# Kernel optimization log

Hardware: AMD Instinct MI355X
Metric: run time of the kernel (lower is better)

The kernel has to match this reference:

```python
import jax, jax.numpy as jnp
import numpy as np

NUM_EMBEDDINGS = 1024
EMBEDDING_DIM = 128
COMMITMENT_COEF = 0.25
DECAY = 0.99
EPS = 1e-5


def setup_inputs() -> dict:
    key = jax.random.key(0)
    k1, k2 = jax.random.split(key)
    z_e = jax.random.normal(k1, (64, EMBEDDING_DIM, 32, 32), dtype=jnp.float32)
    lim = 1.0 / NUM_EMBEDDINGS
    embed = jax.random.uniform(k2, (NUM_EMBEDDINGS, EMBEDDING_DIM), dtype=jnp.float32,
                               minval=-lim, maxval=lim)
    ema_cluster_size = jnp.zeros((NUM_EMBEDDINGS,), dtype=jnp.float32)
    ema_w = embed.copy()  # buffer initialized as clone of embed weights
    return {"z_e": z_e, "embed": embed,
            "ema_cluster_size": ema_cluster_size, "ema_w": ema_w}


def reference(z_e, embed, ema_cluster_size, ema_w):
    B, D, H, W = z_e.shape
    K = embed.shape[0]
    # [B,D,H,W] -> [N,D]
    flat = jnp.transpose(z_e, (0, 2, 3, 1)).reshape(-1, D)
    distances = (jnp.sum(flat ** 2, axis=1, keepdims=True)
                 + jnp.sum(embed ** 2, axis=1)
                 - 2.0 * jnp.matmul(flat, embed.T))
    encoding_indices = jnp.argmin(distances, axis=1)  # [N]

    quantized = embed[encoding_indices].reshape(B, H, W, D)
    quantized = jnp.transpose(quantized, (0, 3, 1, 2))  # [B,D,H,W]

    # ---- EMA codebook update (training path) ----
    N = flat.shape[0]
    cluster_size = jax.ops.segment_sum(jnp.ones((N,), flat.dtype),
                                       encoding_indices, num_segments=K)
    new_ema_cluster_size = DECAY * ema_cluster_size + (1.0 - DECAY) * cluster_size
    dw = jax.ops.segment_sum(flat, encoding_indices, num_segments=K)  # encodings^T @ flat
    new_ema_w = DECAY * ema_w + (1.0 - DECAY) * dw
    n = jnp.sum(new_ema_cluster_size)
    cs = (new_ema_cluster_size + EPS) / (n + K * EPS) * n
    new_embed = new_ema_w / cs[:, None]

    commitment_loss = jnp.mean((jax.lax.stop_gradient(quantized) - z_e) ** 2)
    loss = commitment_loss * COMMITMENT_COEF
    # straight-through estimator
    quantized_st = z_e + jax.lax.stop_gradient(quantized - z_e)
    indices = encoding_indices.reshape(B, H * W)
    return (quantized_st, indices, loss, new_embed, new_ema_cluster_size, new_ema_w)
```

## Files before the change

### kernel.cpp

```cpp
#include <hip/hip_runtime.h>

#define K_CODES 1024
#define DIM 128
#define HW 1024
#define NTOT 65536
#define DECAY 0.99f
#define OMD 0.01f
#define EPS 1e-5f
#define CCOEF 0.25f
#define MARGIN 1e-4f
#define FLCAP 24576

#define OFF_Q    0
#define OFF_IDX  8388608
#define OFF_LOSS (8388608 + 65536)
#define OFF_EMB  (OFF_LOSS + 1)
#define OFF_ECS  (OFF_EMB + 131072)
#define OFF_EMAW (OFF_ECS + 1024)

#define W_NORM2 0
#define W_RCP   1024
#define W_HIST  2048
#define W_LOSS  3072
#define W_FLCNT 3073
#define W_CNT2  3076
#define W_FL    (3076 + 24576)
#define W_M1F   (27652 + 24576)
#define W_CAND  (52228 + 24576)
#define W_EH    (76804 + 196608)
#define W_EL    (273412 + 65536)
#define W_NXIDX (338948 + 65536)
#define W_FLAT  (404484 + 65536)
#define W_NEED  (470020 + 8388608)

typedef __attribute__((ext_vector_type(8))) short short8v;
typedef __attribute__((ext_vector_type(4))) float f32x4;

__device__ __forceinline__ unsigned short f2bf(float f) {
    unsigned u = __float_as_uint(f);
    u += 0x7fffu + ((u >> 16) & 1u);
    return (unsigned short)(u >> 16);
}
__device__ __forceinline__ float bf2f(unsigned short h) {
    return __uint_as_float(((unsigned)h) << 16);
}

__global__ __launch_bounds__(256) void kzero(float* __restrict__ p, int n) {
    int i = blockIdx.x * 256 + threadIdx.x;
    if (i < n) p[i] = 0.f;
}

__device__ __forceinline__ float np_pairwise_sumsq_128(const float* p, size_t stride) {
    float r[8][4];
    #pragma unroll
    for (int j = 0; j < 8; ++j)
        #pragma unroll
        for (int L = 0; L < 4; ++L) {
            float x = p[(size_t)(j * 4 + L) * stride];
            r[j][L] = __fmul_rn(x, x);
        }
    #pragma unroll
    for (int c = 1; c < 4; ++c)
        #pragma unroll
        for (int j = 0; j < 8; ++j)
            #pragma unroll
            for (int L = 0; L < 4; ++L) {
                float x = p[(size_t)(c * 32 + j * 4 + L) * stride];
                r[j][L] = __fadd_rn(r[j][L], __fmul_rn(x, x));
            }
    float V[4];
    #pragma unroll
    for (int L = 0; L < 4; ++L) {
        float a = __fadd_rn(r[0][L], r[1][L]);
        float b = __fadd_rn(r[2][L], r[3][L]);
        float c2 = __fadd_rn(r[4][L], r[5][L]);
        float d2 = __fadd_rn(r[6][L], r[7][L]);
        V[L] = __fadd_rn(__fadd_rn(a, b), __fadd_rn(c2, d2));
    }
    return __fadd_rn(__fadd_rn(V[0], V[1]), __fadd_rn(V[2], V[3]));
}

__global__ __launch_bounds__(256) void knx(const float* __restrict__ ze,
                                           float* __restrict__ nx,
                                           float* __restrict__ flat_c) {
    __shared__ float t[128][133];
    const int tid = threadIdx.x;
    const int n0 = blockIdx.x * 128;
    const int b = n0 >> 10, hw0 = n0 & (HW - 1);
    const float* zb = ze + (size_t)b * (DIM * HW) + hw0;
    #pragma unroll
    for (int i = 0; i < 64; ++i) {
        int d = i * 2 + (tid >> 7);
        int hw = tid & 127;
        t[hw][d] = zb[(size_t)d * HW + hw];
    }
    __syncthreads();
    if (tid < 128) nx[n0 + tid] = np_pairwise_sumsq_128(&t[tid][0], 1);
    if (flat_c) {
        #pragma unroll
        for (int i = 0; i < 16; ++i) {
            int lin = i * 256 + tid;
            int r  = lin >> 5;
            int c4 = lin & 31;
            float4 v = *(const float4*)&t[r][c4 * 4];
            *(float4*)&flat_c[(size_t)(n0 + r) * DIM + c4 * 4] = v;
        }
    }
}

__global__ __launch_bounds__(256) void knorm(const float* __restrict__ embed,
                                             float* __restrict__ norm2,
                                             unsigned short* __restrict__ eh_g,
                                             unsigned short* __restrict__ el_g) {
    int k = blockIdx.x * 256 + threadIdx.x;
    const float* row = embed + (size_t)k * DIM;
    norm2[k] = np_pairwise_sumsq_128(row, 1);
    if (eh_g) {
        #pragma unroll 8
        for (int d = 0; d < DIM; ++d) {
            float f = row[d];
            unsigned short h = f2bf(f);
            eh_g[(size_t)k * DIM + d] = h;
            el_g[(size_t)k * DIM + d] = f2bf(f - bf2f(h));
        }
    }
}

__global__ __launch_bounds__(256, 4) void kapprox(
    const float* __restrict__ flat_c, const unsigned short* __restrict__ eh_g,
    const unsigned short* __restrict__ el_g, const float* __restrict__ norm2,
    int* __restrict__ idx_ws, float* __restrict__ idx_out,
    unsigned* __restrict__ hist, unsigned* __restrict__ flcnt,
    unsigned* __restrict__ fl_list, float* __restrict__ m1f)
{
    __shared__ __align__(16) unsigned short ehs[2][32 * 128];
    __shared__ __align__(16) unsigned short els[2][32 * 128];
    __shared__ float nes[1024];

    const int tid = threadIdx.x;
    const int l = tid & 63;
    const int w = tid >> 6;
    const int lg = l >> 4;
    const int lm = l & 15;
    const int n0 = blockIdx.x * 64;

    for (int i = tid; i < 1024; i += 256) nes[i] = norm2[i];

    short8v xh[4], xl[4];
    {
        const float* xr = flat_c + (size_t)(n0 + w * 16 + lm) * DIM;
        #pragma unroll
        for (int ks = 0; ks < 4; ++ks) {
            int kb = ks * 32 + lg * 8;
            float f0[8];
            *(float4*)&f0[0] = *(const float4*)(xr + kb);
            *(float4*)&f0[4] = *(const float4*)(xr + kb + 4);
            #pragma unroll
            for (int e = 0; e < 8; ++e) {
                unsigned short h0 = f2bf(f0[e]);
                xh[ks][e] = (short)h0;
                xl[ks][e] = (short)f2bf(f0[e] - bf2f(h0));
            }
        }
    }

    const int c0g = tid >> 4;
    const int g0  = tid & 15;
    const int c1g = 16 + c0g;
    const int so0 = c0g * 128 + ((g0 ^ (c0g & 15)) * 8);
    const int so1 = c1g * 128 + ((g0 ^ (c1g & 15)) * 8);
    const size_t gsrc0 = (size_t)c0g * 128 + g0 * 8;
    const size_t gsrc1 = (size_t)c1g * 128 + g0 * 8;

    int roff[4];
    #pragma unroll
    for (int ks = 0; ks < 4; ++ks)
        roff[ks] = lm * 128 + (((ks * 4 + lg) ^ lm) * 8);

    uint4 peh0 = *(const uint4*)(eh_g + gsrc0);
    uint4 peh1 = *(const uint4*)(eh_g + gsrc1);
    uint4 pel0 = *(const uint4*)(el_g + gsrc0);
    uint4 pel1 = *(const uint4*)(el_g + gsrc1);
    *(uint4*)&ehs[0][so0] = peh0;
    *(uint4*)&ehs[0][so1] = peh1;
    *(uint4*)&els[0][so0] = pel0;
    *(uint4*)&els[0][so1] = pel1;
    __syncthreads();

    float m1 = 3.4e38f, m2 = 3.4e38f;
    int c1 = 0;

    for (int it = 0; it < 32; ++it) {
        const int ct = it;
        const int buf = it & 1;
        const int nt = it + 1;
        if (nt < 32) {
            const size_t nb = (size_t)nt * (32 * 128);
            peh0 = *(const uint4*)(eh_g + nb + gsrc0);
            peh1 = *(const uint4*)(eh_g + nb + gsrc1);
            pel0 = *(const uint4*)(el_g + nb + gsrc0);
            pel1 = *(const uint4*)(el_g + nb + gsrc1);
        }
        f32x4 a00 = {0.f,0.f,0.f,0.f}, a01 = {0.f,0.f,0.f,0.f};
        const unsigned short* be = &ehs[buf][0];
        const unsigned short* bl = &els[buf][0];
        #pragma unroll
        for (int ks = 0; ks < 4; ++ks) {
            short8v eA = *(const short8v*)(be + roff[ks]);
            short8v lA = *(const short8v*)(bl + roff[ks]);
            short8v eB = *(const short8v*)(be + 2048 + roff[ks]);
            short8v lB = *(const short8v*)(bl + 2048 + roff[ks]);
            a00 = __builtin_amdgcn_mfma_f32_16x16x32_bf16(eA, xh[ks], a00, 0, 0, 0);
            a00 = __builtin_amdgcn_mfma_f32_16x16x32_bf16(lA, xh[ks], a00, 0, 0, 0);
            a00 = __builtin_amdgcn_mfma_f32_16x16x32_bf16(eA, xl[ks], a00, 0, 0, 0);
            a01 = __builtin_amdgcn_mfma_f32_16x16x32_bf16(eB, xh[ks], a01, 0, 0, 0);
            a01 = __builtin_amdgcn_mfma_f32_16x16x32_bf16(lB, xh[ks], a01, 0, 0, 0);
            a01 = __builtin_amdgcn_mfma_f32_16x16x32_bf16(eB, xl[ks], a01, 0, 0, 0);
        }
        #pragma unroll
        for (int r = 0; r < 4; ++r) {
            int code0 = ct * 32 + lg * 4 + r;
            int code1 = code0 + 16;
            float s0 = nes[code0] - 2.f * a00[r];
            float s1 = nes[code1] - 2.f * a01[r];
            m2 = fminf(m2, fmaxf(m1, s0));
            if (s0 < m1) { m1 = s0; c1 = code0; }
            m2 = fminf(m2, fmaxf(m1, s1));
            if (s1 < m1) { m1 = s1; c1 = code1; }
        }
        if (nt < 32) {
            *(uint4*)&ehs[buf ^ 1][so0] = peh0;
            *(uint4*)&ehs[buf ^ 1][so1] = peh1;
            *(uint4*)&els[buf ^ 1][so0] = pel0;
            *(uint4*)&els[buf ^ 1][so1] = pel1;
        }
        __syncthreads();
    }

    #pragma unroll
    for (int mk = 16; mk <= 32; mk <<= 1) {
        float om1 = __shfl_xor(m1, mk, 64);
        int   oc1 = __shfl_xor(c1, mk, 64);
        float om2 = __shfl_xor(m2, mk, 64);
        m2 = fminf(fminf(m2, om2), fmaxf(m1, om1));
        if (om1 < m1 || (om1 == m1 && oc1 < c1)) { m1 = om1; c1 = oc1; }
    }
    if (lg == 0) {
        int n = n0 + w * 16 + lm;
        if (m2 - m1 > MARGIN) {
            idx_ws[n] = c1;
            idx_out[n] = (float)c1;
            atomicAdd(&hist[c1], 1u);
        } else {
            unsigned p = atomicAdd(flcnt, 1u);
            if (p < FLCAP) { fl_list[p] = (unsigned)n; m1f[p] = m1; }
            else {
                idx_ws[n] = c1; idx_out[n] = (float)c1;
                atomicAdd(&hist[c1], 1u);
            }
        }
    }
}

__global__ __launch_bounds__(256, 2) void kapprox2(
    const float* __restrict__ flat_c, const unsigned short* __restrict__ eh_g,
    const unsigned short* __restrict__ el_g, const float* __restrict__ norm2,
    const float* __restrict__ m1f, const unsigned* __restrict__ flcnt,
    const unsigned* __restrict__ fl_list, unsigned* __restrict__ cnt_g,
    unsigned* __restrict__ cand_g)
{
    __shared__ __align__(16) unsigned short ehs[2][32 * 128];
    __shared__ __align__(16) unsigned short els[2][32 * 128];
    __shared__ float nes[1024];
    __shared__ unsigned ccnt[128];
    __shared__ unsigned ccode[128][8];
    __shared__ int rid[128];
    __shared__ float thrs[128];

    const int tid = threadIdx.x;
    const int l = tid & 63;
    const int w = tid >> 6;
    const int lg = l >> 4;
    const int lm = l & 15;

    for (int i = tid; i < 1024; i += 256) nes[i] = norm2[i];

    const int c0g = tid >> 4;
    const int g0  = tid & 15;
    const int c1g = 16 + c0g;
    const int so0 = c0g * 128 + ((g0 ^ (c0g & 15)) * 8);
    const int so1 = c1g * 128 + ((g0 ^ (c1g & 15)) * 8);
    const size_t gsrc0 = (size_t)c0g * 128 + g0 * 8;
    const size_t gsrc1 = (size_t)c1g * 128 + g0 * 8;

    int roff[4];
    #pragma unroll
    for (int ks = 0; ks < 4; ++ks)
        roff[ks] = lm * 128 + (((ks * 4 + lg) ^ lm) * 8);

    unsigned nflag = flcnt[0];
    if (nflag > FLCAP) nflag = FLCAP;
    const unsigned nbat = (nflag + 127u) >> 7;
    const unsigned nwork = nbat * 8u;

    for (unsigned wi = blockIdx.x; wi < nwork; wi += gridDim.x) {
        const unsigned bat = wi >> 3;
        const int cq = (int)(wi & 7u);
        __syncthreads();
        if (tid < 128) {
            unsigned p = bat * 128u + tid;
            int n = (p < nflag) ? (int)fl_list[p] : -1;
            rid[tid] = n;
            thrs[tid] = (n >= 0) ? m1f[p] + MARGIN : -3.4e38f;
            ccnt[tid] = 0;
        }
        __syncthreads();

        const int lr0 = w * 32 + lm, lr1 = lr0 + 16;
        const int nr0 = rid[lr0], nr1 = rid[lr1];
        const float thr0 = thrs[lr0], thr1 = thrs[lr1];
        short8v xh0[4], xl0[4], xh1[4], xl1[4];
        {
            const float* xr0 = flat_c + (size_t)(nr0 < 0 ? 0 : nr0) * DIM;
            const float* xr1 = flat_c + (size_t)(nr1 < 0 ? 0 : nr1) * DIM;
            #pragma unroll
            for (int ks = 0; ks < 4; ++ks) {
                int kb = ks * 32 + lg * 8;
                float f0[8], f1[8];
                *(float4*)&f0[0] = *(const float4*)(xr0 + kb);
                *(float4*)&f0[4] = *(const float4*)(xr0 + kb + 4);
                *(float4*)&f1[0] = *(const float4*)(xr1 + kb);
                *(float4*)&f1[4] = *(const float4*)(xr1 + kb + 4);
                #pragma unroll
                for (int e = 0; e < 8; ++e) {
                    unsigned short h0 = f2bf(f0[e]);
                    unsigned short h1 = f2bf(f1[e]);
                    xh0[ks][e] = (short)h0;
                    xl0[ks][e] = (short)f2bf(f0[e] - bf2f(h0));
                    xh1[ks][e] = (short)h1;
                    xl1[ks][e] = (short)f2bf(f1[e] - bf2f(h1));
                }
            }
        }

        const int it0 = cq * 4;
        {
            const size_t nb = (size_t)it0 * (32 * 128);
            uint4 a = *(const uint4*)(eh_g + nb + gsrc0);
            uint4 b = *(const uint4*)(eh_g + nb + gsrc1);
            uint4 c = *(const uint4*)(el_g + nb + gsrc0);
            uint4 d = *(const uint4*)(el_g + nb + gsrc1);
            *(uint4*)&ehs[0][so0] = a;
            *(uint4*)&ehs[0][so1] = b;
            *(uint4*)&els[0][so0] = c;
            *(uint4*)&els[0][so1] = d;
        }
        __syncthreads();

        uint4 peh0, peh1, pel0, pel1;
        for (int ii = 0; ii < 4; ++ii) {
            const int it = it0 + ii;
            const int buf = ii & 1;
            if (ii + 1 < 4) {
                const size_t nb = (size_t)(it + 1) * (32 * 128);
                peh0 = *(const uint4*)(eh_g + nb + gsrc0);
                peh1 = *(const uint4*)(eh_g + nb + gsrc1);
                pel0 = *(const uint4*)(el_g + nb + gsrc0);
                pel1 = *(const uint4*)(el_g + nb + gsrc1);
            }
            f32x4 a00 = {0.f,0.f,0.f,0.f}, a01 = {0.f,0.f,0.f,0.f};
            f32x4 a10 = {0.f,0.f,0.f,0.f}, a11 = {0.f,0.f,0.f,0.f};
            const unsigned short* be = &ehs[buf][0];
            const unsigned short* bl = &els[buf][0];
            #pragma unroll
            for (int ks = 0; ks < 4; ++ks) {
                short8v eA = *(const short8v*)(be + roff[ks]);
                short8v lA = *(const short8v*)(bl + roff[ks]);
                short8v eB = *(const short8v*)(be + 2048 + roff[ks]);
                short8v lB = *(const short8v*)(bl + 2048 + roff[ks]);
                a00 = __builtin_amdgcn_mfma_f32_16x16x32_bf16(eA, xh0[ks], a00, 0, 0, 0);
                a00 = __builtin_amdgcn_mfma_f32_16x16x32_bf16(lA, xh0[ks], a00, 0, 0, 0);
                a00 = __builtin_amdgcn_mfma_f32_16x16x32_bf16(eA, xl0[ks], a00, 0, 0, 0);
                a10 = __builtin_amdgcn_mfma_f32_16x16x32_bf16(eA, xh1[ks], a10, 0, 0, 0);
                a10 = __builtin_amdgcn_mfma_f32_16x16x32_bf16(lA, xh1[ks], a10, 0, 0, 0);
                a10 = __builtin_amdgcn_mfma_f32_16x16x32_bf16(eA, xl1[ks], a10, 0, 0, 0);
                a01 = __builtin_amdgcn_mfma_f32_16x16x32_bf16(eB, xh0[ks], a01, 0, 0, 0);
                a01 = __builtin_amdgcn_mfma_f32_16x16x32_bf16(lB, xh0[ks], a01, 0, 0, 0);
                a01 = __builtin_amdgcn_mfma_f32_16x16x32_bf16(eB, xl0[ks], a01, 0, 0, 0);
                a11 = __builtin_amdgcn_mfma_f32_16x16x32_bf16(eB, xh1[ks], a11, 0, 0, 0);
                a11 = __builtin_amdgcn_mfma_f32_16x16x32_bf16(lB, xh1[ks], a11, 0, 0, 0);
                a11 = __builtin_amdgcn_mfma_f32_16x16x32_bf16(eB, xl1[ks], a11, 0, 0, 0);
            }
            #pragma unroll
            for (int r = 0; r < 4; ++r) {
                int code0 = it * 32 + lg * 4 + r;
                int code1 = code0 + 16;
                float s00 = nes[code0] - 2.f * a00[r];
                float s01 = nes[code1] - 2.f * a01[r];
                float s10 = nes[code0] - 2.f * a10[r];
                float s11 = nes[code1] - 2.f * a11[r];
                if (s00 <= thr0) {
                    unsigned p = atomicAdd(&ccnt[lr0], 1u);
                    if (p < 8) ccode[lr0][p] = (unsigned)code0;
                }
                if (s01 <= thr0) {
                    unsigned p = atomicAdd(&ccnt[lr0], 1u);
                    if (p < 8) ccode[lr0][p] = (unsigned)code1;
                }
                if (s10 <= thr1) {
                    unsigned p = atomicAdd(&ccnt[lr1], 1u);
                    if (p < 8) ccode[lr1][p] = (unsigned)code0;
                }
                if (s11 <= thr1) {
                    unsigned p = atomicAdd(&ccnt[lr1], 1u);
                    if (p < 8) ccode[lr1][p] = (unsigned)code1;
                }
            }
            if (ii + 1 < 4) {
                *(uint4*)&ehs[buf ^ 1][so0] = peh0;
                *(uint4*)&ehs[buf ^ 1][so1] = peh1;
                *(uint4*)&els[buf ^ 1][so0] = pel0;
                *(uint4*)&els[buf ^ 1][so1] = pel1;
            }
            __syncthreads();
        }

        if (tid < 128) {
            int n = rid[tid];
            unsigned lc = ccnt[tid];
            if (lc > 8u) lc = 8u;
            if (n >= 0 && lc > 0) {
                unsigned p = bat * 128u + tid;
                unsigned base = atomicAdd(&cnt_g[p], lc);
                for (unsigned j = 0; j < lc; ++j) {
                    unsigned slot = base + j;
                    if (slot < 8u) cand_g[(size_t)p * 8 + slot] = ccode[tid][j];
                }
            }
        }
    }
}

__global__ __launch_bounds__(256) void krescore(
    const float* __restrict__ flat_c, const float* __restrict__ embed,
    const float* __restrict__ norm2, const float* nxg,
    const unsigned* __restrict__ flcnt, const unsigned* __restrict__ fl_list,
    const unsigned* __restrict__ cnt_g, const unsigned* __restrict__ cand_g,
    int* idx_ws, float* __restrict__ idx_out, unsigned* __restrict__ hist)
{
    unsigned nflag = flcnt[0];
    if (nflag > FLCAP) nflag = FLCAP;
    for (unsigned p = blockIdx.x * 256u + threadIdx.x; p < nflag;
         p += gridDim.x * 256u) {
        const int n = (int)fl_list[p];
        unsigned c = cnt_g[p];
        if (c > 8u) c = 8u;
        unsigned cc[8];
        uint4 pk0 = *(const uint4*)(cand_g + (size_t)p * 8);
        uint4 pk1 = *(const uint4*)(cand_g + (size_t)p * 8 + 4);
        cc[0] = pk0.x; cc[1] = pk0.y; cc[2] = pk0.z; cc[3] = pk0.w;
        cc[4] = pk1.x; cc[5] = pk1.y; cc[6] = pk1.z; cc[7] = pk1.w;
        int bestk = (int)cc[0];
        if (c > 1) {
            float bests = 3.4e38f;
            bestk = 1 << 30;
            const float* xr = flat_c + (size_t)n * DIM;
            const float nx = nxg[n];
            #pragma unroll
            for (int q = 0; q < 8; ++q) {
                if (q < (int)c) {
                    int k = (int)cc[q];
                    const float* er = embed + (size_t)k * DIM;
                    float dot = 0.f;
                    #pragma unroll
                    for (int d4 = 0; d4 < 32; ++d4) {
                        float4 e4 = *(const float4*)(er + d4 * 4);
                        float4 x4 = *(const float4*)(xr + d4 * 4);
                        dot = fmaf(x4.x, e4.x, dot);
                        dot = fmaf(x4.y, e4.y, dot);
                        dot = fmaf(x4.z, e4.z, dot);
                        dot = fmaf(x4.w, e4.w, dot);
                    }
                    float qv = __fadd_rn(nx, norm2[k]);
                    float s = __fsub_rn(qv, __fmul_rn(2.f, dot));
                    if (s < bests || (s == bests && k < bestk)) { bests = s; bestk = k; }
                }
            }
        }
        idx_ws[n] = bestk;
        idx_out[n] = (float)bestk;
        atomicAdd(&hist[bestk], 1u);
    }
}

__global__ __launch_bounds__(256, 2) void kargmin(
    const float* __restrict__ ze, const float* __restrict__ embed,
    const float* __restrict__ norm2, const float* nxg,
    int* idx_ws, float* __restrict__ idx_out,
    unsigned int* __restrict__ hist)
{
    __shared__ float xs[128 * 36];
    __shared__ float es[128 * 36];
    __shared__ float nxs[128];
    const int tid = threadIdx.x;
    const int tx = tid & 15, ty = tid >> 4;
    const int n0 = blockIdx.x * 128;
    const float* zbase = ze + (size_t)(n0 >> 10) * (DIM * HW) + (n0 & (HW - 1));
    if (tid < 128) nxs[tid] = nxg[n0 + tid];
    float minv[8];
    int   mini[8];
    #pragma unroll
    for (int i = 0; i < 8; ++i) { minv[i] = 3.4e38f; mini[i] = 0; }
    for (int kt = 0; kt < 8; ++kt) {
        float acc[8][8];
        #pragma unroll
        for (int i = 0; i < 8; ++i)
            #pragma unroll
            for (int j = 0; j < 8; ++j) acc[i][j] = 0.f;
        for (int dc = 0; dc < 4; ++dc) {
            __syncthreads();
            #pragma unroll
            for (int it = 0; it < 4; ++it) {
                int lin = it * 256 + tid;
                int r  = lin & 127;
                int gu = lin >> 7;
                const float* gp = zbase + (size_t)(dc * 32 + gu * 4) * HW + r;
                float4 v;
                v.x = gp[0]; v.y = gp[HW]; v.z = gp[2 * HW]; v.w = gp[3 * HW];
                *(float4*)&xs[r * 36 + gu * 4] = v;
            }
            #pragma unroll
            for (int it = 0; it < 4; ++it) {
                int lin = it * 256 + tid;
                int k  = lin >> 3;
                int gu = lin & 7;
                float4 v = *(const float4*)(embed + (size_t)(kt * 128 + k) * DIM + dc * 32 + gu * 4);
                *(float4*)&es[k * 36 + gu * 4] = v;
            }
            __syncthreads();
            #pragma unroll
            for (int g = 0; g < 8; ++g) {
                float4 xf[8];
                #pragma unroll
                for (int i = 0; i < 8; ++i)
                    xf[i] = *(const float4*)&xs[(ty + i * 16) * 36 + g * 4];
                #pragma unroll
                for (int j = 0; j < 8; ++j) {
                    float4 ef = *(const float4*)&es[(tx + j * 16) * 36 + g * 4];
                    #pragma unroll
                    for (int i = 0; i < 8; ++i) {
                        acc[i][j] = fmaf(xf[i].x, ef.x, acc[i][j]);
                        acc[i][j] = fmaf(xf[i].y, ef.y, acc[i][j]);
                        acc[i][j] = fmaf(xf[i].z, ef.z, acc[i][j]);
                        acc[i][j] = fmaf(xf[i].w, ef.w, acc[i][j]);
                    }
                }
            }
        }
        #pragma unroll
        for (int j = 0; j < 8; ++j) {
            int kg = kt * 128 + tx + j * 16;
            float nrm = norm2[kg];
            #pragma unroll
            for (int i = 0; i < 8; ++i) {
                float q = __fadd_rn(nxs[ty + i * 16], nrm);
                float t = __fmul_rn(2.f, acc[i][j]);
                float s = __fsub_rn(q, t);
                if (s < minv[i]) { minv[i] = s; mini[i] = kg; }
            }
        }
    }
    #pragma unroll
    for (int i = 0; i < 8; ++i) {
        float v = minv[i]; int ix = mini[i];
        #pragma unroll
        for (int off = 8; off >= 1; off >>= 1) {
            float v2 = __shfl_xor(v, off, 16);
            int   i2 = __shfl_xor(ix, off, 16);
            if (v2 < v || (v2 == v && i2 < ix)) { v = v2; ix = i2; }
        }
        if (tx == 0) {
            int n = n0 + ty + i * 16;
            idx_ws[n] = ix;
            idx_out[n] = (float)ix;
            atomicAdd(&hist[ix], 1u);
        }
    }
}

__global__ __launch_bounds__(256) void kquant(
    const float* __restrict__ ze, const float* __restrict__ embed,
    const int* __restrict__ idx_ws, float* __restrict__ qout,
    float* __restrict__ dw_atomic, float* __restrict__ loss_acc)
{
    __shared__ float q[128 * 133];
    __shared__ int idxs[128];
    __shared__ float lsum[4];
    const int tid = threadIdx.x;
    const int n0 = blockIdx.x * 128;
    const int b = n0 >> 10;
    const int hw0 = n0 & (HW - 1);
    if (tid < 128) idxs[tid] = idx_ws[n0 + tid];
    __syncthreads();
    #pragma unroll
    for (int it = 0; it < 16; ++it) {
        int r = it * 8 + (tid >> 5);
        int c = tid & 31;
        float4 v = *(const float4*)(embed + (size_t)idxs[r] * DIM + c * 4);
        *(float4*)&q[r * 133 + c * 4] = v;
    }
    __syncthreads();
    const float* zb = ze + (size_t)b * (DIM * HW) + hw0;
    float* qb = qout + (size_t)b * (DIM * HW) + hw0;
    float lacc = 0.f;
    for (int dd = 0; dd < 64; ++dd) {
        int d = dd * 2 + (tid >> 7);
        int hw = tid & 127;
        float val = q[hw * 133 + d];
        size_t off = (size_t)d * HW + hw;
        float z = zb[off];
        qb[off] = val;
        float diff = val - z;
        lacc = fmaf(diff, diff, lacc);
        if (dw_atomic) atomicAdd(&dw_atomic[idxs[hw] * DIM + d], z);
    }
    #pragma unroll
    for (int off = 32; off >= 1; off >>= 1) lacc += __shfl_xor(lacc, off, 64);
    if ((tid & 63) == 0) lsum[tid >> 6] = lacc;
    __syncthreads();
    if (tid == 0) atomicAdd(loss_acc, lsum[0] + lsum[1] + lsum[2] + lsum[3]);
}

__global__ __launch_bounds__(512) void kdwf(
    const int* __restrict__ idx_ws, const float* __restrict__ flat_c,
    const float* __restrict__ ema_w, const float* __restrict__ rcp,
    float* __restrict__ out_emb, float* __restrict__ out_emaw)
{
    __shared__ float part[8][128];
    const int k = blockIdx.x;
    const int lane = threadIdx.x & 63;
    const int w = threadIdx.x >> 6;
    float lo = 0.f, hi = 0.f;
    const int nbeg = w * (NTOT / 8);
    const int nend = nbeg + (NTOT / 8);
    for (int base = nbeg; base < nend; base += 64) {
        int my = idx_ws[base + lane];
        unsigned long long m = __ballot(my == k);
        while (m) {
            int bit = __ffsll((long long)m) - 1;
            m &= m - 1;
            const float* row = flat_c + (size_t)(base + bit) * DIM;
            lo += row[lane];
            hi += row[lane + 64];
        }
    }
    part[w][lane] = lo;
    part[w][lane + 64] = hi;
    __syncthreads();
    if (w == 0) {
        float a = part[0][lane], b = part[0][lane + 64];
        #pragma unroll
        for (int u = 1; u < 8; ++u) {
            a += part[u][lane];
            b += part[u][lane + 64];
        }
        const float r = rcp[k];
        int elo = k * DIM + lane, ehi = elo + 64;
        float nwa = DECAY * ema_w[elo] + OMD * a;
        float nwb = DECAY * ema_w[ehi] + OMD * b;
        out_emaw[elo] = nwa;
        out_emaw[ehi] = nwb;
        out_emb[elo] = nwa * r;
        out_emb[ehi] = nwb * r;
    }
}

__global__ __launch_bounds__(256) void kfin1(
    const unsigned int* __restrict__ hist, const float* __restrict__ ema_cs,
    float* __restrict__ out_ecs, float* __restrict__ rcp,
    float* __restrict__ loss_out, const float* __restrict__ loss_acc)
{
    const int tid = threadIdx.x;
    __shared__ float wsum[4];
    float local = 0.f;
    float necs[4];
    #pragma unroll
    for (int u = 0; u < 4; ++u) {
        int k = u * 256 + tid;
        necs[u] = DECAY * ema_cs[k] + OMD * (float)hist[k];
        out_ecs[k] = necs[u];
        local += necs[u];
    }
    #pragma unroll
    for (int off = 32; off >= 1; off >>= 1) local += __shfl_xor(local, off, 64);
    if ((tid & 63) == 0) wsum[tid >> 6] = local;
    __syncthreads();
    float ntot = wsum[0] + wsum[1] + wsum[2] + wsum[3];
    #pragma unroll
    for (int u = 0; u < 4; ++u) {
        int k = u * 256 + tid;
        float cs = (necs[u] + EPS) / (ntot + (float)K_CODES * EPS) * ntot;
        rcp[k] = 1.f / cs;
    }
    if (tid == 0) loss_out[0] = loss_acc[0] * (CCOEF / (float)((size_t)NTOT * DIM));
}

__global__ __launch_bounds__(256) void kfin2(
    const float* __restrict__ ema_w, const float* __restrict__ dw,
    const float* __restrict__ rcp, float* __restrict__ out_emb,
    float* __restrict__ out_emaw)
{
    int e = blockIdx.x * 256 + threadIdx.x;
    int k = e >> 7;
    float nw = DECAY * ema_w[e] + OMD * dw[e];
    out_emaw[e] = nw;
    out_emb[e] = nw * rcp[k];
}

extern "C" void kernel_launch(void* const* d_in, const int* in_sizes, int n_in,
                              void* d_out, int out_size, void* d_ws, size_t ws_size,
                              hipStream_t stream) {
    const float* ze     = (const float*)d_in[0];
    const float* embed  = (const float*)d_in[1];
    const float* ema_cs = (const float*)d_in[2];
    const float* ema_w  = (const float*)d_in[3];
    float* out = (float*)d_out;

    float* ws = (float*)d_ws;
    float*          ws_norm2 = ws + W_NORM2;
    float*          ws_rcp   = ws + W_RCP;
    unsigned*       ws_hist  = (unsigned*)(ws + W_HIST);
    float*          ws_loss  = ws + W_LOSS;
    unsigned*       ws_flcnt = (unsigned*)(ws + W_FLCNT);
    unsigned*       ws_cnt   = (unsigned*)(ws + W_CNT2);
    unsigned*       ws_fl    = (unsigned*)(ws + W_FL);
    float*          ws_m1    = ws + W_M1F;
    unsigned*       ws_cand  = (unsigned*)(ws + W_CAND);
    float*          ws_dw    = ws + W_CAND;
    unsigned short* ws_eh    = (unsigned short*)(ws + W_EH);
    unsigned short* ws_el    = (unsigned short*)(ws + W_EL);
    float*          ws_nx    = ws + W_NXIDX;
    int*            ws_idx   = (int*)(ws + W_NXIDX);
    float*          ws_flat  = ws + W_FLAT;
    const size_t need = (size_t)W_NEED * sizeof(float);
    const bool big_ws = ws_size >= need;

    if (big_ws) {
        hipLaunchKernelGGL(kzero, dim3(101), dim3(256), 0, stream, (float*)ws_hist, 25604);
        hipLaunchKernelGGL(knx, dim3(512), dim3(256), 0, stream, ze, ws_nx, ws_flat);
        hipLaunchKernelGGL(knorm, dim3(4), dim3(256), 0, stream, embed, ws_norm2, ws_eh, ws_el);
        hipLaunchKernelGGL(kapprox, dim3(1024), dim3(256), 0, stream,
                           ws_flat, ws_eh, ws_el, ws_norm2,
                           ws_idx, out + OFF_IDX, ws_hist, ws_flcnt, ws_fl, ws_m1);
        hipLaunchKernelGGL(kapprox2, dim3(512), dim3(256), 0, stream,
                           ws_flat, ws_eh, ws_el, ws_norm2,
                           ws_m1, ws_flcnt, ws_fl, ws_cnt, ws_cand);
        hipLaunchKernelGGL(krescore, dim3(64), dim3(256), 0, stream,
                           ws_flat, embed, ws_norm2, ws_nx, ws_flcnt, ws_fl,
                           ws_cnt, ws_cand, ws_idx, out + OFF_IDX, ws_hist);
        hipLaunchKernelGGL(kquant, dim3(512), dim3(256), 0, stream,
                           ze, embed, ws_idx, out + OFF_Q, (float*)nullptr, ws_loss);
        hipLaunchKernelGGL(kfin1, dim3(1), dim3(256), 0, stream,
                           ws_hist, ema_cs, out + OFF_ECS, ws_rcp, out + OFF_LOSS, ws_loss);
        hipLaunchKernelGGL(kdwf, dim3(1024), dim3(512), 0, stream,
                           ws_idx, ws_flat, ema_w, ws_rcp,
                           out + OFF_EMB, out + OFF_EMAW);
    } else {
        hipLaunchKernelGGL(kzero, dim3(5), dim3(256), 0, stream, (float*)ws_hist, 1028);
        hipLaunchKernelGGL(kzero, dim3(512), dim3(256), 0, stream, ws_dw, 131072);
        hipLaunchKernelGGL(knx, dim3(512), dim3(256), 0, stream, ze, ws_nx, (float*)nullptr);
        hipLaunchKernelGGL(knorm, dim3(4), dim3(256), 0, stream, embed, ws_norm2,
                           (unsigned short*)nullptr, (unsigned short*)nullptr);
        hipLaunchKernelGGL(kargmin, dim3(512), dim3(256), 0, stream,
                           ze, embed, ws_norm2, ws_nx, ws_idx, out + OFF_IDX, ws_hist);
        hipLaunchKernelGGL(kquant, dim3(512), dim3(256), 0, stream,
                           ze, embed, ws_idx, out + OFF_Q, ws_dw, ws_loss);
        hipLaunchKernelGGL(kfin1, dim3(1), dim3(256), 0, stream,
                           ws_hist, ema_cs, out + OFF_ECS, ws_rcp, out + OFF_LOSS, ws_loss);
        hipLaunchKernelGGL(kfin2, dim3(512), dim3(256), 0, stream,
                           ema_w, ws_dw, ws_rcp, out + OFF_EMB, out + OFF_EMAW);
    }
}
```

Measured before the change: 194.7 us.

## Pre-swizzle codebook in prep kernel and stage tiles via direct global-to-LDS loads

Replaces the 4-block knorm kernel and the kzero launch with a single 128-block kprep kernel. It zeroes the workspace, computes the code norms with wave shuffles, and writes the bf16 hi/lo codebook already in the XOR-swizzled LDS layout. kapprox and kapprox2 then stage codebook tiles with global_load_lds, which removes the register round trip and the explicit LDS stores from the double-buffer loop. The norm reduction order changes, which could perturb tie-breaking. It also relies on async LDS writes being complete at the existing barriers.

```diff
diff --git a/kernel.cpp b/kernel.cpp
--- a/kernel.cpp
+++ b/kernel.cpp
@@ -45,6 +45,12 @@
     return __uint_as_float(((unsigned)h) << 16);
 }
 
+__device__ __forceinline__ void gl16(const void* g, void* l) {
+    __builtin_amdgcn_global_load_lds(
+        (const __attribute__((address_space(1))) unsigned int*)g,
+        (__attribute__((address_space(3))) unsigned int*)l, 16, 0, 0);
+}
+
 __global__ __launch_bounds__(256) void kzero(float* __restrict__ p, int n) {
     int i = blockIdx.x * 256 + threadIdx.x;
     if (i < n) p[i] = 0.f;
@@ -78,6 +84,50 @@
         V[L] = __fadd_rn(__fadd_rn(a, b), __fadd_rn(c2, d2));
     }
     return __fadd_rn(__fadd_rn(V[0], V[1]), __fadd_rn(V[2], V[3]));
+}
+
+__global__ __launch_bounds__(256) void kprep(
+    const float* __restrict__ embed, float* __restrict__ norm2,
+    unsigned short* __restrict__ ehs_g, unsigned short* __restrict__ els_g,
+    float* __restrict__ zero_p, int zero_n)
+{
+    const int tid = threadIdx.x;
+    const int bid = blockIdx.x;
+    int zi = bid * 256 + tid;
+    if (zi < zero_n) zero_p[zi] = 0.f;
+    {
+        const int g32 = tid >> 5, l32 = tid & 31;
+        const int k = bid * 8 + g32;
+        const float* row = embed + (size_t)k * DIM;
+        float x = row[l32];
+        float r = __fmul_rn(x, x);
+        #pragma unroll
+        for (int c = 1; c < 4; ++c) {
+            float y = row[c * 32 + l32];
+            r = __fadd_rn(r, __fmul_rn(y, y));
+        }
+        float s1 = __fadd_rn(r, __shfl_xor(r, 4, 64));
+        float s2 = __fadd_rn(s1, __shfl_xor(s1, 8, 64));
+        float s3 = __fadd_rn(s2, __shfl_xor(s2, 16, 64));
+        float h1 = __fadd_rn(s3, __shfl_xor(s3, 1, 64));
+        float h2 = __fadd_rn(h1, __shfl_xor(h1, 2, 64));
+        if (l32 == 0) norm2[k] = h2;
+    }
+    if (ehs_g) {
+        int hu = bid * 256 + tid;
+        int U = hu >> 1, half = hu & 1;
+        int code = U >> 4;
+        int g = (U & 15) ^ (code & 15);
+        const float* src = embed + (size_t)code * DIM + g * 8 + half * 4;
+        float4 f = *(const float4*)src;
+        unsigned short a = f2bf(f.x), b = f2bf(f.y), c = f2bf(f.z), d = f2bf(f.w);
+        ushort4 hi; hi.x = a; hi.y = b; hi.z = c; hi.w = d;
+        ushort4 lo;
+        lo.x = f2bf(f.x - bf2f(a)); lo.y = f2bf(f.y - bf2f(b));
+        lo.z = f2bf(f.z - bf2f(c)); lo.w = f2bf(f.w - bf2f(d));
+        *(ushort4*)(ehs_g + (size_t)U * 8 + half * 4) = hi;
+        *(ushort4*)(els_g + (size_t)U * 8 + half * 4) = lo;
+    }
 }
 
 __global__ __launch_bounds__(256) void knx(const float* __restrict__ ze,
@@ -108,24 +158,6 @@
     }
 }
 
-__global__ __launch_bounds__(256) void knorm(const float* __restrict__ embed,
-                                             float* __restrict__ norm2,
-                                             unsigned short* __restrict__ eh_g,
-                                             unsigned short* __restrict__ el_g) {
-    int k = blockIdx.x * 256 + threadIdx.x;
-    const float* row = embed + (size_t)k * DIM;
-    norm2[k] = np_pairwise_sumsq_128(row, 1);
-    if (eh_g) {
-        #pragma unroll 8
-        for (int d = 0; d < DIM; ++d) {
-            float f = row[d];
-            unsigned short h = f2bf(f);
-            eh_g[(size_t)k * DIM + d] = h;
-            el_g[(size_t)k * DIM + d] = f2bf(f - bf2f(h));
-        }
-    }
-}
-
 __global__ __launch_bounds__(256, 4) void kapprox(
     const float* __restrict__ flat_c, const unsigned short* __restrict__ eh_g,
     const unsigned short* __restrict__ el_g, const float* __restrict__ norm2,
@@ -164,42 +196,37 @@
         }
     }
 
-    const int c0g = tid >> 4;
-    const int g0  = tid & 15;
-    const int c1g = 16 + c0g;
-    const int so0 = c0g * 128 + ((g0 ^ (c0g & 15)) * 8);
-    const int so1 = c1g * 128 + ((g0 ^ (c1g & 15)) * 8);
-    const size_t gsrc0 = (size_t)c0g * 128 + g0 * 8;
-    const size_t gsrc1 = (size_t)c1g * 128 + g0 * 8;
-
     int roff[4];
     #pragma unroll
     for (int ks = 0; ks < 4; ++ks)
         roff[ks] = lm * 128 + (((ks * 4 + lg) ^ lm) * 8);
 
-    uint4 peh0 = *(const uint4*)(eh_g + gsrc0);
-    uint4 peh1 = *(const uint4*)(eh_g + gsrc1);
-    uint4 pel0 = *(const uint4*)(el_g + gsrc0);
-    uint4 pel1 = *(const uint4*)(el_g + gsrc1);
-    *(uint4*)&ehs[0][so0] = peh0;
-    *(uint4*)&ehs[0][so1] = peh1;
-    *(uint4*)&els[0][so0] = pel0;
-    *(uint4*)&els[0][so1] = pel1;
+    const int woff = w * 2048 + l * 16;
+    const int lws  = w * 2048;
+
+    {
+        const char* gh = (const char*)eh_g + woff;
+        const char* gl = (const char*)el_g + woff;
+        char* lh = (char*)&ehs[0][0] + lws;
+        char* ll = (char*)&els[0][0] + lws;
+        gl16(gh, lh);          gl16(gh + 1024, lh + 1024);
+        gl16(gl, ll);          gl16(gl + 1024, ll + 1024);
+    }
     __syncthreads();
 
     float m1 = 3.4e38f, m2 = 3.4e38f;
     int c1 = 0;
 
     for (int it = 0; it < 32; ++it) {
-        const int ct = it;
         const int buf = it & 1;
-        const int nt = it + 1;
-        if (nt < 32) {
-            const size_t nb = (size_t)nt * (32 * 128);
-            peh0 = *(const uint4*)(eh_g + nb + gsrc0);
-            peh1 = *(const uint4*)(eh_g + nb + gsrc1);
-            pel0 = *(const uint4*)(el_g + nb + gsrc0);
-            pel1 = *(const uint4*)(el_g + nb + gsrc1);
+        if (it + 1 < 32) {
+            const size_t nb = (size_t)(it + 1) * 8192;
+            const char* gh = (const char*)eh_g + nb + woff;
+            const char* gl = (const char*)el_g + nb + woff;
+            char* lh = (char*)&ehs[buf ^ 1][0] + lws;
+            char* ll = (char*)&els[buf ^ 1][0] + lws;
+            gl16(gh, lh);          gl16(gh + 1024, lh + 1024);
+            gl16(gl, ll);          gl16(gl + 1024, ll + 1024);
         }
         f32x4 a00 = {0.f,0.f,0.f,0.f}, a01 = {0.f,0.f,0.f,0.f};
         const unsigned short* be = &ehs[buf][0];
@@ -219,7 +246,7 @@
         }
         #pragma unroll
         for (int r = 0; r < 4; ++r) {
-            int code0 = ct * 32 + lg * 4 + r;
+            int code0 = it * 32 + lg * 4 + r;
             int code1 = code0 + 16;
             float s0 = nes[code0] - 2.f * a00[r];
             float s1 = nes[code1] - 2.f * a01[r];
@@ -227,12 +254,6 @@
             if (s0 < m1) { m1 = s0; c1 = code0; }
             m2 = fminf(m2, fmaxf(m1, s1));
             if (s1 < m1) { m1 = s1; c1 = code1; }
-        }
-        if (nt < 32) {
-            *(uint4*)&ehs[buf ^ 1][so0] = peh0;
-            *(uint4*)&ehs[buf ^ 1][so1] = peh1;
-            *(uint4*)&els[buf ^ 1][so0] = pel0;
-            *(uint4*)&els[buf ^ 1][so1] = pel1;
         }
         __syncthreads();
     }
@@ -285,18 +306,13 @@
 
     for (int i = tid; i < 1024; i += 256) nes[i] = norm2[i];
 
-    const int c0g = tid >> 4;
-    const int g0  = tid & 15;
-    const int c1g = 16 + c0g;
-    const int so0 = c0g * 128 + ((g0 ^ (c0g & 15)) * 8);
-    const int so1 = c1g * 128 + ((g0 ^ (c1g & 15)) * 8);
-    const size_t gsrc0 = (size_t)c0g * 128 + g0 * 8;
-    const size_t gsrc1 = (size_t)c1g * 128 + g0 * 8;
-
     int roff[4];
     #pragma unroll
     for (int ks = 0; ks < 4; ++ks)
         roff[ks] = lm * 128 + (((ks * 4 + lg) ^ lm) * 8);
+
+    const int woff = w * 2048 + l * 16;
+    const int lws  = w * 2048;
 
     unsigned nflag = flcnt[0];
     if (nflag > FLCAP) nflag = FLCAP;
@@ -345,28 +361,27 @@
 
         const int it0 = cq * 4;
         {
-            const size_t nb = (size_t)it0 * (32 * 128);
-            uint4 a = *(const uint4*)(eh_g + nb + gsrc0);
-            uint4 b = *(const uint4*)(eh_g + nb + gsrc1);
-            uint4 c = *(const uint4*)(el_g + nb + gsrc0);
-            uint4 d = *(const uint4*)(el_g + nb + gsrc1);
-            *(uint4*)&ehs[0][so0] = a;
-            *(uint4*)&ehs[0][so1] = b;
-            *(uint4*)&els[0][so0] = c;
-            *(uint4*)&els[0][so1] = d;
+            const size_t nb = (size_t)it0 * 8192;
+            const char* gh = (const char*)eh_g + nb + woff;
+            const char* gl = (const char*)el_g + nb + woff;
+            char* lh = (char*)&ehs[0][0] + lws;
+            char* ll = (char*)&els[0][0] + lws;
+            gl16(gh, lh);          gl16(gh + 1024, lh + 1024);
+            gl16(gl, ll);          gl16(gl + 1024, ll + 1024);
         }
         __syncthreads();
 
-        uint4 peh0, peh1, pel0, pel1;
         for (int ii = 0; ii < 4; ++ii) {
             const int it = it0 + ii;
             const int buf = ii & 1;
             if (ii + 1 < 4) {
-                const size_t nb = (size_t)(it + 1) * (32 * 128);
-                peh0 = *(const uint4*)(eh_g + nb + gsrc0);
-                peh1 = *(const uint4*)(eh_g + nb + gsrc1);
-                pel0 = *(const uint4*)(el_g + nb + gsrc0);
-                pel1 = *(const uint4*)(el_g + nb + gsrc1);
+                const size_t nb = (size_t)(it + 1) * 8192;
+                const char* gh = (const char*)eh_g + nb + woff;
+                const char* gl = (const char*)el_g + nb + woff;
+                char* lh = (char*)&ehs[buf ^ 1][0] + lws;
+                char* ll = (char*)&els[buf ^ 1][0] + lws;
+                gl16(gh, lh);          gl16(gh + 1024, lh + 1024);
+                gl16(gl, ll);          gl16(gl + 1024, ll + 1024);
             }
             f32x4 a00 = {0.f,0.f,0.f,0.f}, a01 = {0.f,0.f,0.f,0.f};
             f32x4 a10 = {0.f,0.f,0.f,0.f}, a11 = {0.f,0.f,0.f,0.f};
@@ -416,12 +431,6 @@
                     if (p < 8) ccode[lr1][p] = (unsigned)code1;
                 }
             }
-            if (ii + 1 < 4) {
-                *(uint4*)&ehs[buf ^ 1][so0] = peh0;
-                *(uint4*)&ehs[buf ^ 1][so1] = peh1;
-                *(uint4*)&els[buf ^ 1][so0] = pel0;
-                *(uint4*)&els[buf ^ 1][so1] = pel1;
-            }
             __syncthreads();
         }
 
@@ -746,9 +755,9 @@
     const bool big_ws = ws_size >= need;
 
     if (big_ws) {
-        hipLaunchKernelGGL(kzero, dim3(101), dim3(256), 0, stream, (float*)ws_hist, 25604);
+        hipLaunchKernelGGL(kprep, dim3(128), dim3(256), 0, stream,
+                           embed, ws_norm2, ws_eh, ws_el, (float*)ws_hist, 25604);
         hipLaunchKernelGGL(knx, dim3(512), dim3(256), 0, stream, ze, ws_nx, ws_flat);
-        hipLaunchKernelGGL(knorm, dim3(4), dim3(256), 0, stream, embed, ws_norm2, ws_eh, ws_el);
         hipLaunchKernelGGL(kapprox, dim3(1024), dim3(256), 0, stream,
                            ws_flat, ws_eh, ws_el, ws_norm2,
                            ws_idx, out + OFF_IDX, ws_hist, ws_flcnt, ws_fl, ws_m1);
@@ -766,11 +775,11 @@
                            ws_idx, ws_flat, ema_w, ws_rcp,
                            out + OFF_EMB, out + OFF_EMAW);
     } else {
-        hipLaunchKernelGGL(kzero, dim3(5), dim3(256), 0, stream, (float*)ws_hist, 1028);
+        hipLaunchKernelGGL(kprep, dim3(128), dim3(256), 0, stream,
+                           embed, ws_norm2, (unsigned short*)nullptr,
+                           (unsigned short*)nullptr, (float*)ws_hist, 1028);
         hipLaunchKernelGGL(kzero, dim3(512), dim3(256), 0, stream, ws_dw, 131072);
         hipLaunchKernelGGL(knx, dim3(512), dim3(256), 0, stream, ze, ws_nx, (float*)nullptr);
-        hipLaunchKernelGGL(knorm, dim3(4), dim3(256), 0, stream, embed, ws_norm2,
-                           (unsigned short*)nullptr, (unsigned short*)nullptr);
         hipLaunchKernelGGL(kargmin, dim3(512), dim3(256), 0, stream,
                            ze, embed, ws_norm2, ws_nx, ws_idx, out + OFF_IDX, ws_hist);
         hipLaunchKernelGGL(kquant, dim3(512), dim3(256), 0, stream,
```

Result: faster. 189.9 us (-2.5%).
